# Optimization experiments

Hardware: AMD Instinct MI355X
Metric: run time of the kernel (lower is better)

The kernel has to match this reference:

```python
import jax, jax.numpy as jnp
import numpy as np

DY, DO, DI = 16, 256, 256
BS = 4096
EPS = 1e-6


def setup_inputs() -> dict:
    key = jax.random.key(0)
    k1, k2, k3, k4, k5 = jax.random.split(key, 5)
    k = 1.0 / float(np.sqrt(DY * DI))
    return {
        "x": jax.random.normal(k1, (DY * DI, BS), dtype=jnp.float32),
        "rms_params": jnp.ones((DY * DI,), dtype=jnp.float32)
        + 0.01 * jax.random.normal(k2, (DY * DI,), dtype=jnp.float32),
        "w_upper": jax.random.uniform(k3, (DY, DO, DI), minval=-k, maxval=k, dtype=jnp.float32),
        "w_lower": jax.random.uniform(k4, (DY, DO, DI), minval=-k, maxval=k, dtype=jnp.float32),
        "bias": jax.random.uniform(k5, (DY * DO,), minval=-k, maxval=k, dtype=jnp.float32),
    }


def reference(x, rms_params, w_upper, w_lower, bias):
    # x: (dy*di, bs) features-first layout, matching the torch op.
    dy, do, di = w_upper.shape
    bs = x.shape[1]
    # Per-column RMS factor (fc in the original op is shape (bs,)).
    fc = jax.lax.rsqrt(jnp.mean(x * x, axis=0) + EPS)  # (bs,)
    xn = x * rms_params[:, None] * fc[None, :]          # fused norm+scale
    xb = xn.reshape(dy, di, bs)
    # Dyadic structured matmul: upper acts on block d, lower on its paired
    # (reversed) block dy-1-d.
    up = jnp.einsum("doi,dib->dob", w_upper, xb)
    lo = jnp.einsum("doi,dib->dob", w_lower, xb[::-1])
    y = jax.nn.relu(up + lo + bias.reshape(dy, do, 1))
    return y.reshape(dy * do, bs)
```

## Files before the change

kernel.cpp:

```cpp
#include <hip/hip_runtime.h>

#define DYN 16
#define DON 256
#define DIN 256
#define BSN 4096
#define NF 4096
#define KTOT 512

typedef unsigned short u16;
typedef __attribute__((ext_vector_type(8))) short bf16x8;
typedef __attribute__((ext_vector_type(4))) float f32x4;
typedef __attribute__((ext_vector_type(4))) unsigned short u16x4;

static __device__ __forceinline__ u16 f2bf(float f) {
  unsigned u = __builtin_bit_cast(unsigned, f);
  u += 0x7fffu + ((u >> 16) & 1u);
  return (u16)(u >> 16);
}
static __device__ __forceinline__ float bf2f(u16 h) {
  unsigned u = ((unsigned)h) << 16;
  return __builtin_bit_cast(float, u);
}

__global__ __launch_bounds__(256) void k_prep_w(
    const float* __restrict__ wu, const float* __restrict__ wl,
    const float* __restrict__ rms, u16* __restrict__ aprep) {
  int e = blockIdx.x * 256 + threadIdx.x;
  int row = e >> 6;
  int k0 = (e & 63) << 3;
  int d = row >> 8;
  const float* src;
  const float* rp;
  if (k0 < 256) {
    src = wu + (size_t)row * 256 + k0;
    rp  = rms + d * 256 + k0;
  } else {
    src = wl + (size_t)row * 256 + (k0 - 256);
    rp  = rms + (DYN - 1 - d) * 256 + (k0 - 256);
  }
  float4 s0 = *reinterpret_cast<const float4*>(src);
  float4 s1 = *reinterpret_cast<const float4*>(src + 4);
  float4 r0 = *reinterpret_cast<const float4*>(rp);
  float4 r1 = *reinterpret_cast<const float4*>(rp + 4);
  bf16x8 o;
  o[0] = (short)f2bf(s0.x * r0.x); o[1] = (short)f2bf(s0.y * r0.y);
  o[2] = (short)f2bf(s0.z * r0.z); o[3] = (short)f2bf(s0.w * r0.w);
  o[4] = (short)f2bf(s1.x * r1.x); o[5] = (short)f2bf(s1.y * r1.y);
  o[6] = (short)f2bf(s1.z * r1.z); o[7] = (short)f2bf(s1.w * r1.w);
  *reinterpret_cast<bf16x8*>(aprep + (size_t)row * KTOT + k0) = o;
}

__global__ __launch_bounds__(256) void k_transpose(
    const float* __restrict__ x, u16* __restrict__ xbf,
    float* __restrict__ partial) {
  __shared__ u16 tile[128 * 132];
  const int t = threadIdx.x;
  const int bt = blockIdx.x, ft = blockIdx.y;
  const float* xb = x + (size_t)ft * 128 * BSN + bt * 128;
  const int frow = t >> 5, b4 = (t & 31) * 4;
  #pragma unroll
  for (int p = 0; p < 16; ++p) {
    int f = p * 8 + frow;
    float4 v = *reinterpret_cast<const float4*>(xb + (size_t)f * BSN + b4);
    u16x4 h;
    h[0] = f2bf(v.x); h[1] = f2bf(v.y); h[2] = f2bf(v.z); h[3] = f2bf(v.w);
    *reinterpret_cast<u16x4*>(&tile[f * 132 + b4]) = h;
  }
  __syncthreads();
  const int chunk = t & 15;
  const int bg = t >> 4;
  #pragma unroll
  for (int p = 0; p < 8; ++p) {
    int b = bg + p * 16;
    float s = 0.f;
    bf16x8 w;
    #pragma unroll
    for (int jj = 0; jj < 8; ++jj) {
      int j = (jj + chunk) & 7;
      u16 v = tile[(chunk * 8 + j) * 132 + b];
      float xv = bf2f(v);
      s += xv * xv;
      w[j] = (short)v;
    }
    *reinterpret_cast<bf16x8*>(
        xbf + (size_t)(bt * 128 + b) * NF + ft * 128 + chunk * 8) = w;
    #pragma unroll
    for (int m = 1; m < 16; m <<= 1) s += __shfl_xor(s, m, 64);
    if (chunk == 0) partial[ft * BSN + bt * 128 + b] = s;
  }
}

__global__ __launch_bounds__(256) void k_fc(
    const float* __restrict__ partial, float* __restrict__ fc) {
  int b = blockIdx.x * 256 + threadIdx.x;
  float s = 0.f;
  #pragma unroll
  for (int i = 0; i < 32; ++i) s += partial[i * BSN + b];
  fc[b] = rsqrtf(s * (1.0f / 4096.0f) + 1e-6f);
}

__global__ __launch_bounds__(512, 2) void k_gemm(
    const u16* __restrict__ aprep, const u16* __restrict__ xbf,
    const float* __restrict__ fc, const float* __restrict__ bias,
    float* __restrict__ out) {
  extern __shared__ u16 lds[];
  u16* As = lds;
  u16* Bs = lds + 3 * 8192;
  const int bid = blockIdx.x;
  const int xcd = bid & 7, w = bid >> 3;
  const int d = (w & 1) ? (15 - xcd) : xcd;
  const int nt = w >> 1;
  const int t = threadIdx.x;
  const int wave = t >> 6, lane = t & 63;
  const int lhi = lane >> 4, llo = lane & 15;
  const int wm = wave >> 2, wn = wave & 3;
  const int arow0 = d * 256;
  const int bcol0 = nt * 256;

  f32x4 acc[8][4] = {};

  auto stage = [&](int slot, int kt) {
    const int fbase = (kt < 8) ? (d * 256 + kt * 32)
                               : ((DYN - 1 - d) * 256 + (kt - 8) * 32);
    #pragma unroll
    for (int j = 0; j < 2; ++j) {
      int c = j * 512 + t;
      int cl = c ^ ((c >> 3) & 7);
      int r = cl >> 2, kc = cl & 3;
      const u16* ga = aprep + (size_t)(arow0 + r) * KTOT + kt * 32 + kc * 8;
      const u16* gb = xbf + (size_t)(bcol0 + r) * NF + fbase + kc * 8;
      unsigned lbase = (unsigned)((j * 512 + wave * 64) * 16);
      __builtin_amdgcn_global_load_lds(
          (const __attribute__((address_space(1))) unsigned int*)ga,
          (__attribute__((address_space(3))) unsigned int*)(
              (char*)&As[slot * 8192] + lbase), 16, 0, 0);
      __builtin_amdgcn_global_load_lds(
          (const __attribute__((address_space(1))) unsigned int*)gb,
          (__attribute__((address_space(3))) unsigned int*)(
              (char*)&Bs[slot * 8192] + lbase), 16, 0, 0);
    }
  };

  const int kmask = ((llo >> 1) & 7) << 4;

  stage(0, 0);
  stage(1, 1);
  asm volatile("s_waitcnt vmcnt(4)\n\ts_barrier" ::: "memory");

  for (int kt = 0; kt < 16; ++kt) {
    const int slot = kt % 3;
    if (kt < 14) stage((kt + 2) % 3, kt + 2);

    bf16x8 af[8], bq[4];
    #pragma unroll
    for (int m = 0; m < 8; ++m) {
      int rowa = wm * 128 + m * 16 + llo;
      int offa = (rowa * 64 + lhi * 16) ^ kmask;
      af[m] = *reinterpret_cast<const bf16x8*>(
          (const char*)&As[slot * 8192] + offa);
    }
    #pragma unroll
    for (int n = 0; n < 4; ++n) {
      int rowb = wn * 64 + n * 16 + llo;
      int offb = (rowb * 64 + lhi * 16) ^ kmask;
      bq[n] = *reinterpret_cast<const bf16x8*>(
          (const char*)&Bs[slot * 8192] + offb);
    }
    __builtin_amdgcn_s_setprio(1);
    #pragma unroll
    for (int m = 0; m < 8; ++m)
      #pragma unroll
      for (int n = 0; n < 4; ++n)
        acc[m][n] = __builtin_amdgcn_mfma_f32_16x16x32_bf16(
            af[m], bq[n], acc[m][n], 0, 0, 0);
    __builtin_amdgcn_s_setprio(0);

    if (kt < 14) {
      asm volatile("s_waitcnt vmcnt(4)\n\ts_barrier" ::: "memory");
    } else if (kt == 14) {
      asm volatile("s_waitcnt vmcnt(0)\n\ts_barrier" ::: "memory");
    }
  }

  float fcv[4];
  #pragma unroll
  for (int n = 0; n < 4; ++n) fcv[n] = fc[bcol0 + wn * 64 + n * 16 + llo];
  #pragma unroll
  for (int m = 0; m < 8; ++m) {
    int row0 = arow0 + wm * 128 + m * 16 + lhi * 4;
    float bv[4];
    #pragma unroll
    for (int r = 0; r < 4; ++r) bv[r] = bias[row0 + r];
    #pragma unroll
    for (int n = 0; n < 4; ++n) {
      int col = bcol0 + wn * 64 + n * 16 + llo;
      #pragma unroll
      for (int r = 0; r < 4; ++r) {
        float v = acc[m][n][r] * fcv[n] + bv[r];
        out[(size_t)(row0 + r) * BSN + col] = fmaxf(v, 0.f);
      }
    }
  }
}

extern "C" void kernel_launch(void* const* d_in, const int* in_sizes, int n_in,
                              void* d_out, int out_size, void* d_ws, size_t ws_size,
                              hipStream_t stream) {
  (void)in_sizes; (void)n_in; (void)out_size; (void)ws_size;
  const float* x    = (const float*)d_in[0];
  const float* rms  = (const float*)d_in[1];
  const float* wu   = (const float*)d_in[2];
  const float* wl   = (const float*)d_in[3];
  const float* bias = (const float*)d_in[4];
  float* out = (float*)d_out;

  char* ws = (char*)d_ws;
  u16* xbf      = (u16*)ws;
  u16* aprep    = (u16*)(ws + 33554432);
  float* partial = (float*)(ws + 37748736);
  float* fc      = (float*)(ws + 38273024);

  k_prep_w<<<1024, 256, 0, stream>>>(wu, wl, rms, aprep);
  k_transpose<<<dim3(32, 32), 256, 0, stream>>>(x, xbf, partial);
  k_fc<<<16, 256, 0, stream>>>(partial, fc);
  k_gemm<<<256, 512, 98304, stream>>>(aprep, xbf, fc, bias, out);
}
```

Baseline: 59.70 us.

## Fuse RMS factor reduction into GEMM and shrink GEMM tiles to 128x128

Removes the separate k_fc launch. Each GEMM block now sums the 32 partial sums for its 128 columns and stores the rsqrt factors in LDS while its first stages load. The GEMM tile drops from 256x256 with 512 threads to 128x128 with 256 threads, so the grid grows from 256 to 1024 blocks and three blocks can fit per CU. This should fill the machine better and save one kernel launch. In exchange, per-block data reuse falls and global/L2 traffic for A and B roughly doubles.

```diff
diff --git a/kernel.cpp b/kernel.cpp
--- a/kernel.cpp
+++ b/kernel.cpp
@@ -90,54 +90,47 @@
   }
 }
 
-__global__ __launch_bounds__(256) void k_fc(
-    const float* __restrict__ partial, float* __restrict__ fc) {
-  int b = blockIdx.x * 256 + threadIdx.x;
-  float s = 0.f;
-  #pragma unroll
-  for (int i = 0; i < 32; ++i) s += partial[i * BSN + b];
-  fc[b] = rsqrtf(s * (1.0f / 4096.0f) + 1e-6f);
-}
-
-__global__ __launch_bounds__(512, 2) void k_gemm(
+__global__ __launch_bounds__(256, 3) void k_gemm(
     const u16* __restrict__ aprep, const u16* __restrict__ xbf,
-    const float* __restrict__ fc, const float* __restrict__ bias,
+    const float* __restrict__ partial, const float* __restrict__ bias,
     float* __restrict__ out) {
-  extern __shared__ u16 lds[];
-  u16* As = lds;
-  u16* Bs = lds + 3 * 8192;
+  extern __shared__ char smem[];
+  float* fcl = (float*)smem;
+  u16* As = (u16*)(smem + 512);
+  u16* Bs = As + 3 * 4096;
   const int bid = blockIdx.x;
-  const int xcd = bid & 7, w = bid >> 3;
-  const int d = (w & 1) ? (15 - xcd) : xcd;
-  const int nt = w >> 1;
+  const int x8 = bid & 7, s = bid >> 3;
+  const int d = (s & 1) ? (15 - x8) : x8;
+  const int mt = (s >> 1) & 1;
+  const int nt = s >> 2;
   const int t = threadIdx.x;
   const int wave = t >> 6, lane = t & 63;
   const int lhi = lane >> 4, llo = lane & 15;
-  const int wm = wave >> 2, wn = wave & 3;
-  const int arow0 = d * 256;
-  const int bcol0 = nt * 256;
-
-  f32x4 acc[8][4] = {};
+  const int wm = wave >> 1, wn = wave & 1;
+  const int arow0 = d * 256 + mt * 128;
+  const int bcol0 = nt * 128;
+
+  f32x4 acc[4][4] = {};
 
   auto stage = [&](int slot, int kt) {
     const int fbase = (kt < 8) ? (d * 256 + kt * 32)
                                : ((DYN - 1 - d) * 256 + (kt - 8) * 32);
     #pragma unroll
     for (int j = 0; j < 2; ++j) {
-      int c = j * 512 + t;
+      int c = j * 256 + t;
       int cl = c ^ ((c >> 3) & 7);
       int r = cl >> 2, kc = cl & 3;
       const u16* ga = aprep + (size_t)(arow0 + r) * KTOT + kt * 32 + kc * 8;
       const u16* gb = xbf + (size_t)(bcol0 + r) * NF + fbase + kc * 8;
-      unsigned lbase = (unsigned)((j * 512 + wave * 64) * 16);
+      unsigned lbase = (unsigned)((j * 256 + wave * 64) * 16);
       __builtin_amdgcn_global_load_lds(
           (const __attribute__((address_space(1))) unsigned int*)ga,
           (__attribute__((address_space(3))) unsigned int*)(
-              (char*)&As[slot * 8192] + lbase), 16, 0, 0);
+              (char*)&As[slot * 4096] + lbase), 16, 0, 0);
       __builtin_amdgcn_global_load_lds(
           (const __attribute__((address_space(1))) unsigned int*)gb,
           (__attribute__((address_space(3))) unsigned int*)(
-              (char*)&Bs[slot * 8192] + lbase), 16, 0, 0);
+              (char*)&Bs[slot * 4096] + lbase), 16, 0, 0);
     }
   };
 
@@ -145,30 +138,37 @@
 
   stage(0, 0);
   stage(1, 1);
+  if (t < 128) {
+    int col = bcol0 + t;
+    float fs = 0.f;
+    #pragma unroll
+    for (int i = 0; i < 32; ++i) fs += partial[i * BSN + col];
+    fcl[t] = rsqrtf(fs * (1.0f / 4096.0f) + 1e-6f);
+  }
   asm volatile("s_waitcnt vmcnt(4)\n\ts_barrier" ::: "memory");
 
   for (int kt = 0; kt < 16; ++kt) {
     const int slot = kt % 3;
     if (kt < 14) stage((kt + 2) % 3, kt + 2);
 
-    bf16x8 af[8], bq[4];
-    #pragma unroll
-    for (int m = 0; m < 8; ++m) {
-      int rowa = wm * 128 + m * 16 + llo;
+    bf16x8 af[4], bq[4];
+    #pragma unroll
+    for (int m = 0; m < 4; ++m) {
+      int rowa = wm * 64 + m * 16 + llo;
       int offa = (rowa * 64 + lhi * 16) ^ kmask;
       af[m] = *reinterpret_cast<const bf16x8*>(
-          (const char*)&As[slot * 8192] + offa);
+          (const char*)&As[slot * 4096] + offa);
     }
     #pragma unroll
     for (int n = 0; n < 4; ++n) {
       int rowb = wn * 64 + n * 16 + llo;
       int offb = (rowb * 64 + lhi * 16) ^ kmask;
       bq[n] = *reinterpret_cast<const bf16x8*>(
-          (const char*)&Bs[slot * 8192] + offb);
+          (const char*)&Bs[slot * 4096] + offb);
     }
     __builtin_amdgcn_s_setprio(1);
     #pragma unroll
-    for (int m = 0; m < 8; ++m)
+    for (int m = 0; m < 4; ++m)
       #pragma unroll
       for (int n = 0; n < 4; ++n)
         acc[m][n] = __builtin_amdgcn_mfma_f32_16x16x32_bf16(
@@ -184,10 +184,10 @@
 
   float fcv[4];
   #pragma unroll
-  for (int n = 0; n < 4; ++n) fcv[n] = fc[bcol0 + wn * 64 + n * 16 + llo];
-  #pragma unroll
-  for (int m = 0; m < 8; ++m) {
-    int row0 = arow0 + wm * 128 + m * 16 + lhi * 4;
+  for (int n = 0; n < 4; ++n) fcv[n] = fcl[wn * 64 + n * 16 + llo];
+  #pragma unroll
+  for (int m = 0; m < 4; ++m) {
+    int row0 = arow0 + wm * 64 + m * 16 + lhi * 4;
     float bv[4];
     #pragma unroll
     for (int r = 0; r < 4; ++r) bv[r] = bias[row0 + r];
@@ -218,10 +218,8 @@
   u16* xbf      = (u16*)ws;
   u16* aprep    = (u16*)(ws + 33554432);
   float* partial = (float*)(ws + 37748736);
-  float* fc      = (float*)(ws + 38273024);
 
   k_prep_w<<<1024, 256, 0, stream>>>(wu, wl, rms, aprep);
   k_transpose<<<dim3(32, 32), 256, 0, stream>>>(x, xbf, partial);
-  k_fc<<<16, 256, 0, stream>>>(partial, fc);
-  k_gemm<<<256, 512, 98304, stream>>>(aprep, xbf, fc, bias, out);
-}
+  k_gemm<<<1024, 256, 49664, stream>>>(aprep, xbf, partial, bias, out);
+}
```

After: 57.87 us. -3.1%, faster.
